# Kernel tuning notes

Hardware: AMD Instinct MI355X
Metric: run time of the kernel (lower is better)

Reference implementation:

```python
import jax, jax.numpy as jnp
import numpy as np

D_NODE = 100
D_HID = 300
EPS = 1e-5


def _gru_step_h0(x, W_ih, b_ih, b_hh):
    # Single torch-GRU step with h0 = 0 (seq len 1), so W_hh @ h0 vanishes
    # and only the hidden biases b_hh survive.
    gi = x @ W_ih.T + b_ih                      # [..., 3*H]
    H = D_HID
    r = jax.nn.sigmoid(gi[..., 0:H] + b_hh[0:H])
    z = jax.nn.sigmoid(gi[..., H:2 * H] + b_hh[H:2 * H])
    n = jnp.tanh(gi[..., 2 * H:3 * H] + r * b_hh[2 * H:3 * H])
    return (1.0 - z) * n                        # h' = (1-z)*n + z*0


def setup_inputs() -> dict:
    key = jax.random.key(0)
    ks = jax.random.split(key, 20)
    B, T, Lq, N = 128, 512, 256, 256
    s = 0.02
    inp = {
        "nodes": jax.random.normal(ks[0], (B * N, D_NODE), jnp.float32),
        "context_rep": jax.random.normal(ks[1], (B, Lq, D_HID), jnp.float32),
        "dia_triples": jax.random.randint(ks[2], (B, T, 3), 0, N, jnp.int64 if jax.config.jax_enable_x64 else jnp.int32),
        "node_number": N,
        # mean_trans: Linear(100, 300)
        "W_mean": s * jax.random.normal(ks[3], (D_HID, D_NODE), jnp.float32),
        "b_mean": jnp.zeros((D_HID,), jnp.float32),
        # bidirectional GRU(300 -> 300); h0=0 so W_hh drops out, keep biases
        "W_ih_f": s * jax.random.normal(ks[4], (3 * D_HID, D_HID), jnp.float32),
        "b_ih_f": s * jax.random.normal(ks[5], (3 * D_HID,), jnp.float32),
        "b_hh_f": s * jax.random.normal(ks[6], (3 * D_HID,), jnp.float32),
        "W_ih_b": s * jax.random.normal(ks[7], (3 * D_HID, D_HID), jnp.float32),
        "b_ih_b": s * jax.random.normal(ks[8], (3 * D_HID,), jnp.float32),
        "b_hh_b": s * jax.random.normal(ks[9], (3 * D_HID,), jnp.float32),
        # output_trans: Linear(600, 300) + tanh
        "W_out": s * jax.random.normal(ks[10], (D_HID, 2 * D_HID), jnp.float32),
        "b_out": jnp.zeros((D_HID,), jnp.float32),
        # trans_node_to_decoder_dim: Linear(100, 300)
        "W_node": s * jax.random.normal(ks[11], (D_HID, D_NODE), jnp.float32),
        "b_node": jnp.zeros((D_HID,), jnp.float32),
        # layernorm(300)
        "gamma": jnp.ones((D_HID,), jnp.float32),
        "beta": jnp.zeros((D_HID,), jnp.float32),
    }
    return inp


def reference(nodes, context_rep, dia_triples, node_number,
              W_mean, b_mean, W_ih_f, b_ih_f, b_hh_f,
              W_ih_b, b_ih_b, b_hh_b, W_out, b_out,
              W_node, b_node, gamma, beta):
    B = context_rep.shape[0]
    N = node_number
    T = dia_triples.shape[1]
    nodes3 = nodes.reshape(B, N, D_NODE)                        # per-dialogue node slices

    # gather head/tail nodes of each triple, mean-aggregate
    head = jnp.broadcast_to(dia_triples[:, :, 0][:, :, None], (B, T, D_NODE))
    tail = jnp.broadcast_to(dia_triples[:, :, -1][:, :, None], (B, T, D_NODE))
    gh = jnp.take_along_axis(nodes3, head, axis=1)              # [B,T,100]
    gt = jnp.take_along_axis(nodes3, tail, axis=1)
    tri_mean = 0.5 * (gh + gt)

    x = tri_mean @ W_mean.T + b_mean                            # [B,T,300] GRU inputs (len-1 paths)

    # bidirectional GRU, one step each direction from h0=0
    h_f = _gru_step_h0(x, W_ih_f, b_ih_f, b_hh_f)
    h_b = _gru_step_h0(x, W_ih_b, b_ih_b, b_hh_b)
    hidden = jnp.concatenate([h_f, h_b], axis=-1)               # [B,T,600]

    hid_ = jnp.tanh(hidden @ W_out.T + b_out)                   # [B,T,300]

    # attention: alpha = softmax(query @ hidden^T, -1).sum(0)
    scores = jnp.einsum("bld,btd->blt", context_rep, hid_)
    alpha = jax.nn.softmax(scores, axis=-1).sum(axis=1)         # [B,T]
    rep = jnp.einsum("bt,btd->bd", alpha, hid_)                 # [B,300]

    mu = rep.mean(axis=-1, keepdims=True)
    var = rep.var(axis=-1, keepdims=True)
    path_feature = (rep - mu) * jax.lax.rsqrt(var + EPS) * gamma + beta
    # dropout is identity in eval mode

    node_feature = nodes3 @ W_node.T + b_node                   # [B,N,300]
    node_mask = jnp.zeros((B, 1, N), dtype=bool)                # equal lengths -> no padding
    return path_feature, node_feature, node_mask
```

## Files before the change

### kernel.cpp

```cpp
#include <hip/hip_runtime.h>
#include <math.h>

#define D_NODE 100
#define D_HID  300
static const int TSEQ = 512, LQn = 256, NNODE = 256;

typedef unsigned int u32;
typedef unsigned short u16;
typedef __attribute__((ext_vector_type(8))) short bf16x8;
typedef __attribute__((ext_vector_type(4))) float f32x4;

__device__ __forceinline__ float bflo(u32 u){ return __uint_as_float(u << 16); }
__device__ __forceinline__ float bfhi(u32 u){ return __uint_as_float(u & 0xffff0000u); }
__device__ __forceinline__ float bf2f(u16 v){ return __uint_as_float(((u32)v) << 16); }
__device__ __forceinline__ u16 f2bf(float f){
    u32 u = __float_as_uint(f);
    return (u16)((u + 0x7fffu + ((u >> 16) & 1u)) >> 16);
}
__device__ __forceinline__ u32 pack_bf(float lo, float hi){
    return ((u32)f2bf(lo)) | (((u32)f2bf(hi)) << 16);
}
__device__ __forceinline__ void gload_lds16(const void* g, void* l){
    __builtin_amdgcn_global_load_lds(
        (const __attribute__((address_space(1))) u32*)g,
        (__attribute__((address_space(3))) u32*)l, 16, 0, 0);
}
__device__ __forceinline__ float fsig(float x){
    return __builtin_amdgcn_rcpf(1.f + __expf(-x));
}
__device__ __forceinline__ float ftanh(float x){
    return 1.f - 2.f*__builtin_amdgcn_rcpf(1.f + __expf(2.f*x));
}

__global__ __launch_bounds__(128)
void k0_prep(const float* __restrict__ Wm, const float* __restrict__ bm,
             const float* __restrict__ Wihf, const float* __restrict__ bihf, const float* __restrict__ bhhf,
             const float* __restrict__ Wihb, const float* __restrict__ bihb, const float* __restrict__ bhhb,
             u16* __restrict__ W4bf, float* __restrict__ bc, float* __restrict__ bhhn)
{
    int j = blockIdx.x, g = blockIdx.y, dir = blockIdx.z;
    int tid = threadIdx.x;
    u16* wout = W4bf + ((size_t)((dir*3+g)*320 + j))*128;
    if (j >= D_HID) {
        wout[tid] = 0;
        if (tid == 0) { bc[(dir*3+g)*320 + j] = 0.f; if (g==2) bhhn[dir*320+j] = 0.f; }
        return;
    }
    const float* Wih = dir ? Wihb : Wihf;
    const float* bih = dir ? bihb : bihf;
    const float* bhh = dir ? bhhb : bhhf;
    const float* wrow = Wih + (size_t)(g*D_HID + j)*D_HID;
    int k = tid;
    float s = 0.f;
    if (k < D_NODE)
        for (int q = 0; q < D_HID; ++q)
            s = fmaf(wrow[q], Wm[q*D_NODE + k], s);
    wout[k] = f2bf(k < D_NODE ? s : 0.f);

    __shared__ float red[128];
    float p = 0.f;
    for (int q = tid; q < D_HID; q += 128) p = fmaf(bm[q], wrow[q], p);
    red[tid] = p;
    __syncthreads();
    for (int off = 64; off > 0; off >>= 1) {
        if (tid < off) red[tid] += red[tid + off];
        __syncthreads();
    }
    if (tid == 0) {
        float base = bih[g*D_HID + j] + red[0];
        if (g < 2) base += bhh[g*D_HID + j];
        bc[(dir*3+g)*320 + j] = base;
        if (g == 2) bhhn[dir*320 + j] = bhh[2*D_HID + j];
    }
}

__global__ __launch_bounds__(256)
void kW(const float* __restrict__ Wout, const float* __restrict__ Wnode,
        u16* __restrict__ Woutbf, u16* __restrict__ Wnbf)
{
    int idx = blockIdx.x*256 + threadIdx.x;
    if (idx < 384*608) {
        int j = idx / 608, k = idx % 608;
        float v = (j < D_HID && k < 600) ? Wout[(size_t)j*600 + k] : 0.f;
        Woutbf[idx] = f2bf(v);
    } else {
        int i2 = idx - 384*608;
        if (i2 < 320*128) {
            int j = i2 >> 7, k = i2 & 127;
            float v = (j < D_HID && k < D_NODE) ? Wnode[(size_t)j*D_NODE + k] : 0.f;
            Wnbf[i2] = f2bf(v);
        }
    }
}

__global__ __launch_bounds__(256)
void kA(const float* __restrict__ nodes, const int* __restrict__ trip,
        u32* __restrict__ Abf, u32* __restrict__ Nbf)
{
    int gid = blockIdx.x*256 + threadIdx.x;
    if (gid < 65536) {
        int b = gid >> 9;
        int hidx = trip[(size_t)gid*3];
        int tidx = trip[(size_t)gid*3 + 2];
        const float4* nh = (const float4*)(nodes + ((size_t)b*NNODE + hidx)*D_NODE);
        const float4* nt = (const float4*)(nodes + ((size_t)b*NNODE + tidx)*D_NODE);
        u32* ar = Abf + (size_t)gid*64;
        #pragma unroll 5
        for (int i = 0; i < 25; ++i) {
            float4 a = nh[i], c = nt[i];
            ar[i*2]   = pack_bf(0.5f*(a.x+c.x), 0.5f*(a.y+c.y));
            ar[i*2+1] = pack_bf(0.5f*(a.z+c.z), 0.5f*(a.w+c.w));
        }
        #pragma unroll
        for (int i = 50; i < 64; ++i) ar[i] = 0;
    } else {
        int r = gid - 65536;
        if (r < 32768) {
            const float4* nr = (const float4*)(nodes + (size_t)r*D_NODE);
            u32* ar = Nbf + (size_t)r*64;
            #pragma unroll 5
            for (int i = 0; i < 25; ++i) {
                float4 a = nr[i];
                ar[i*2]   = pack_bf(a.x, a.y);
                ar[i*2+1] = pack_bf(a.z, a.w);
            }
            #pragma unroll
            for (int i = 50; i < 64; ++i) ar[i] = 0;
        }
    }
}

__global__ __launch_bounds__(256)
void kC(const float* __restrict__ ctx, u32* __restrict__ Cbf)
{
    int idx = blockIdx.x*256 + threadIdx.x;
    int r = idx / 160, cp = idx % 160;
    int col = cp*2;
    u32 v = 0;
    if (col < D_HID) {
        float2 f = *(const float2*)(ctx + (size_t)r*D_HID + col);
        v = pack_bf(f.x, f.y);
    }
    Cbf[(size_t)r*160 + cp] = v;
}

__global__ __launch_bounds__(256)
void k1_gru(const u16* __restrict__ Abf, const u16* __restrict__ W4bf,
            const float* __restrict__ bc, const float* __restrict__ bhhn,
            u16* __restrict__ H)
{
    __shared__ char smem[16384];
    int tid = threadIdx.x;
    int lane = tid & 63, w = tid >> 6;
    int l15 = lane & 15, lq = lane >> 4;
    int m0 = blockIdx.x * 64;
    int dir = blockIdx.y / 5;
    int jg = blockIdx.y % 5;
    int j0w = jg*64 + w*16;

    bf16x8 bfr[3][4];
    const u16* Wb = W4bf + (size_t)dir*3*320*128;
    #pragma unroll
    for (int g = 0; g < 3; ++g)
        #pragma unroll
        for (int ks = 0; ks < 4; ++ks)
            bfr[g][ks] = *(const bf16x8*)(Wb + ((size_t)(g*320 + j0w + l15))*128 + ks*32 + lq*8);

    #pragma unroll
    for (int ks = 0; ks < 4; ++ks) {
        const u16* g = Abf + ((size_t)(m0 + w*16 + l15))*128 + ks*32 + lq*8;
        gload_lds16(g, smem + (size_t)((w*4 + ks)*64)*16);
    }
    __syncthreads();

    f32x4 acc[4][3];
    #pragma unroll
    for (int ms = 0; ms < 4; ++ms)
        #pragma unroll
        for (int g = 0; g < 3; ++g)
            acc[ms][g] = (f32x4){0.f,0.f,0.f,0.f};

    #pragma unroll
    for (int ms = 0; ms < 4; ++ms)
        #pragma unroll
        for (int ks = 0; ks < 4; ++ks) {
            bf16x8 a = *(const bf16x8*)(smem + (size_t)(((ms*4+ks)*64 + lane))*16);
            acc[ms][0] = __builtin_amdgcn_mfma_f32_16x16x32_bf16(a, bfr[0][ks], acc[ms][0], 0,0,0);
            acc[ms][1] = __builtin_amdgcn_mfma_f32_16x16x32_bf16(a, bfr[1][ks], acc[ms][1], 0,0,0);
            acc[ms][2] = __builtin_amdgcn_mfma_f32_16x16x32_bf16(a, bfr[2][ks], acc[ms][2], 0,0,0);
        }

    int j = j0w + l15;
    float bcr = bc[(dir*3+0)*320 + j];
    float bcz = bc[(dir*3+1)*320 + j];
    float bcn = bc[(dir*3+2)*320 + j];
    float bn2 = bhhn[dir*320 + j];
    bool ok = (j < D_HID);
    #pragma unroll
    for (int ms = 0; ms < 4; ++ms)
        #pragma unroll
        for (int i = 0; i < 4; ++i) {
            float r = fsig(acc[ms][0][i] + bcr);
            float z = fsig(acc[ms][1][i] + bcz);
            float n = ftanh(acc[ms][2][i] + bcn + r*bn2);
            float h = (1.f - z)*n;
            if (ok) H[(size_t)(m0 + ms*16 + lq*4 + i)*608 + dir*D_HID + j] = f2bf(h);
        }
}

__global__ __launch_bounds__(256, 2)
void k2_out(const u16* __restrict__ H, const u16* __restrict__ Woutbf,
            const float* __restrict__ bout, u16* __restrict__ Hid)
{
    __shared__ char smem[40960];
    int tid = threadIdx.x;
    int lane = tid & 63, w = tid >> 6;
    int l15 = lane & 15, lq = lane >> 4;
    int m0 = blockIdx.x * 64;
    int j0 = blockIdx.y * 128;
    int jA = j0 + w*16, jB = j0 + 64 + w*16;

    bf16x8 bA[19], bB[19];
    #pragma unroll
    for (int ks = 0; ks < 19; ++ks) {
        bA[ks] = *(const bf16x8*)(Woutbf + ((size_t)(jA + l15))*608 + ks*32 + lq*8);
        bB[ks] = *(const bf16x8*)(Woutbf + ((size_t)(jB + l15))*608 + ks*32 + lq*8);
    }
    f32x4 acc[4][2];
    #pragma unroll
    for (int ms = 0; ms < 4; ++ms) { acc[ms][0] = (f32x4){0,0,0,0}; acc[ms][1] = (f32x4){0,0,0,0}; }

    #pragma unroll
    for (int c = 0; c < 2; ++c) {
        const int kb = c ? 10 : 0;
        const int nks = c ? 9 : 10;
        #pragma unroll
        for (int kk = 0; kk < 10; ++kk)
            if (kk < nks) {
                const u16* g = H + ((size_t)(m0 + w*16 + l15))*608 + (kb+kk)*32 + lq*8;
                gload_lds16(g, smem + (size_t)((w*10 + kk)*64)*16);
            }
        __syncthreads();
        #pragma unroll
        for (int ms = 0; ms < 4; ++ms)
            #pragma unroll
            for (int kk = 0; kk < 10; ++kk)
                if (kk < nks) {
                    bf16x8 a = *(const bf16x8*)(smem + (size_t)(((ms*10+kk)*64 + lane))*16);
                    acc[ms][0] = __builtin_amdgcn_mfma_f32_16x16x32_bf16(a, bA[kb+kk], acc[ms][0], 0,0,0);
                    acc[ms][1] = __builtin_amdgcn_mfma_f32_16x16x32_bf16(a, bB[kb+kk], acc[ms][1], 0,0,0);
                }
        __syncthreads();
    }

    #pragma unroll
    for (int jj = 0; jj < 2; ++jj) {
        int j = (jj ? jB : jA) + l15;
        if (j < 320) {
            bool real = (j < D_HID);
            float bo = real ? bout[j] : 0.f;
            #pragma unroll
            for (int ms = 0; ms < 4; ++ms)
                #pragma unroll
                for (int i = 0; i < 4; ++i) {
                    u16 v = real ? f2bf(ftanh(acc[ms][jj][i] + bo)) : (u16)0;
                    Hid[(size_t)(m0 + ms*16 + lq*4 + i)*320 + j] = v;
                }
        }
    }
}

__global__ __launch_bounds__(256, 2)
void k3_attn(const u16* __restrict__ Cbf, const u16* __restrict__ Hid,
             float* __restrict__ alphap)
{
    __shared__ char smemA[4096];
    __shared__ char smemB[32768];
    __shared__ float rmax[64*4], rsum[64*4];
    int tid = threadIdx.x;
    int lane = tid & 63, w = tid >> 6;
    int l15 = lane & 15, lq = lane >> 4;
    int b = blockIdx.y;
    int mblk = blockIdx.x;
    const u16* Ab = Cbf + ((size_t)b*LQn + mblk*64)*320;
    const u16* Bb = Hid + ((size_t)b*TSEQ)*320;

    f32x4 acc[4][8];
    #pragma unroll
    for (int ms = 0; ms < 4; ++ms)
        #pragma unroll
        for (int g = 0; g < 8; ++g)
            acc[ms][g] = (f32x4){0,0,0,0};

    for (int ks = 0; ks < 10; ++ks) {
        gload_lds16(Ab + ((size_t)(w*16 + l15))*320 + ks*32 + lq*8,
                    smemA + (size_t)(w*64)*16);
        #pragma unroll
        for (int i = 0; i < 8; ++i) {
            int nt = w*8 + i;
            gload_lds16(Bb + ((size_t)(nt*16 + l15))*320 + ks*32 + lq*8,
                        smemB + (size_t)(nt*64)*16);
        }
        __syncthreads();
        bf16x8 afr[4];
        #pragma unroll
        for (int ms = 0; ms < 4; ++ms)
            afr[ms] = *(const bf16x8*)(smemA + (size_t)((ms*64 + lane))*16);
        #pragma unroll
        for (int i = 0; i < 8; ++i) {
            bf16x8 bfr = *(const bf16x8*)(smemB + (size_t)(((w*8+i)*64 + lane))*16);
            #pragma unroll
            for (int ms = 0; ms < 4; ++ms)
                acc[ms][i] = __builtin_amdgcn_mfma_f32_16x16x32_bf16(afr[ms], bfr, acc[ms][i], 0,0,0);
        }
        __syncthreads();
    }

    #pragma unroll
    for (int ms = 0; ms < 4; ++ms)
        #pragma unroll
        for (int i = 0; i < 4; ++i) {
            float m = acc[ms][0][i];
            #pragma unroll
            for (int g = 1; g < 8; ++g) m = fmaxf(m, acc[ms][g][i]);
            m = fmaxf(m, __shfl_xor(m, 1));
            m = fmaxf(m, __shfl_xor(m, 2));
            m = fmaxf(m, __shfl_xor(m, 4));
            m = fmaxf(m, __shfl_xor(m, 8));
            if (l15 == 0) rmax[(ms*16 + lq*4 + i)*4 + w] = m;
        }
    __syncthreads();
    float mfin[4][4];
    #pragma unroll
    for (int ms = 0; ms < 4; ++ms)
        #pragma unroll
        for (int i = 0; i < 4; ++i) {
            float4 mv = *(const float4*)&rmax[(ms*16 + lq*4 + i)*4];
            mfin[ms][i] = fmaxf(fmaxf(mv.x, mv.y), fmaxf(mv.z, mv.w));
        }
    #pragma unroll
    for (int ms = 0; ms < 4; ++ms)
        #pragma unroll
        for (int i = 0; i < 4; ++i) {
            float s = 0.f;
            #pragma unroll
            for (int g = 0; g < 8; ++g) {
                float e = __expf(acc[ms][g][i] - mfin[ms][i]);
                acc[ms][g][i] = e;
                s += e;
            }
            s += __shfl_xor(s, 1);
            s += __shfl_xor(s, 2);
            s += __shfl_xor(s, 4);
            s += __shfl_xor(s, 8);
            if (l15 == 0) rsum[(ms*16 + lq*4 + i)*4 + w] = s;
        }
    __syncthreads();
    float inv[4][4];
    #pragma unroll
    for (int ms = 0; ms < 4; ++ms)
        #pragma unroll
        for (int i = 0; i < 4; ++i) {
            float4 sv = *(const float4*)&rsum[(ms*16 + lq*4 + i)*4];
            inv[ms][i] = __builtin_amdgcn_rcpf(sv.x + sv.y + sv.z + sv.w);
        }
    float* ap = alphap + ((size_t)b*4 + mblk)*TSEQ;
    #pragma unroll
    for (int g = 0; g < 8; ++g) {
        float c = 0.f;
        #pragma unroll
        for (int ms = 0; ms < 4; ++ms)
            #pragma unroll
            for (int i = 0; i < 4; ++i)
                c = fmaf(acc[ms][g][i], inv[ms][i], c);
        c += __shfl_xor(c, 16);
        c += __shfl_xor(c, 32);
        if (lq == 0) ap[w*128 + g*16 + l15] = c;
    }
}

__global__ __launch_bounds__(320)
void k4_rep(const float* __restrict__ alphap, const u16* __restrict__ Hid,
            const float* __restrict__ gamma, const float* __restrict__ beta,
            float* __restrict__ outP)
{
    __shared__ float al[512];
    __shared__ float rs[5], rss[5];
    int tid = threadIdx.x, b = blockIdx.x;
    const float* ap = alphap + (size_t)b*4*TSEQ;
    for (int i = tid; i < 512; i += 320)
        al[i] = ap[i] + ap[512 + i] + ap[1024 + i] + ap[1536 + i];
    __syncthreads();
    float acc = 0.f;
    if (tid < D_HID) {
        const u16* hp = Hid + (size_t)b*TSEQ*320 + tid;
        #pragma unroll 8
        for (int t = 0; t < TSEQ; ++t)
            acc = fmaf(al[t], bf2f(hp[(size_t)t*320]), acc);
    }
    float v = (tid < D_HID) ? acc : 0.f;
    float s = v, q = v*v;
    #pragma unroll
    for (int off = 32; off > 0; off >>= 1) { s += __shfl_xor(s, off, 64); q += __shfl_xor(q, off, 64); }
    if ((tid & 63) == 0) { rs[tid >> 6] = s; rss[tid >> 6] = q; }
    __syncthreads();
    float S = rs[0]+rs[1]+rs[2]+rs[3]+rs[4];
    float Q = rss[0]+rss[1]+rss[2]+rss[3]+rss[4];
    float mu = S * (1.f/300.f);
    float var = Q * (1.f/300.f) - mu*mu;
    if (tid < D_HID)
        outP[(size_t)b*D_HID + tid] = (acc - mu) * rsqrtf(var + 1e-5f) * gamma[tid] + beta[tid];
}

__global__ __launch_bounds__(256)
void k5_node(const u16* __restrict__ Nbf, const u16* __restrict__ Wnbf,
             const float* __restrict__ bn, float* __restrict__ outN)
{
    __shared__ char smem[16384];
    int tid = threadIdx.x;
    int lane = tid & 63, w = tid >> 6;
    int l15 = lane & 15, lq = lane >> 4;
    int m0 = blockIdx.x * 64;
    int j0w = blockIdx.y*64 + w*16;

    bf16x8 bw[4];
    #pragma unroll
    for (int ks = 0; ks < 4; ++ks)
        bw[ks] = *(const bf16x8*)(Wnbf + ((size_t)(j0w + l15))*128 + ks*32 + lq*8);

    #pragma unroll
    for (int ks = 0; ks < 4; ++ks) {
        const u16* g = Nbf + ((size_t)(m0 + w*16 + l15))*128 + ks*32 + lq*8;
        gload_lds16(g, smem + (size_t)((w*4 + ks)*64)*16);
    }
    __syncthreads();

    f32x4 acc[4];
    #pragma unroll
    for (int ms = 0; ms < 4; ++ms) acc[ms] = (f32x4){0,0,0,0};
    #pragma unroll
    for (int ms = 0; ms < 4; ++ms)
        #pragma unroll
        for (int ks = 0; ks < 4; ++ks) {
            bf16x8 a = *(const bf16x8*)(smem + (size_t)(((ms*4+ks)*64 + lane))*16);
            acc[ms] = __builtin_amdgcn_mfma_f32_16x16x32_bf16(a, bw[ks], acc[ms], 0,0,0);
        }

    int j = j0w + l15;
    if (j < D_HID) {
        float bo = bn[j];
        #pragma unroll
        for (int ms = 0; ms < 4; ++ms)
            #pragma unroll
            for (int i = 0; i < 4; ++i)
                outN[(size_t)(m0 + ms*16 + lq*4 + i)*D_HID + j] = acc[ms][i] + bo;
    }
}

extern "C" void kernel_launch(void* const* d_in, const int* in_sizes, int n_in,
                              void* d_out, int out_size, void* d_ws, size_t ws_size,
                              hipStream_t stream) {
    const float* nodes  = (const float*)d_in[0];
    const float* ctx    = (const float*)d_in[1];
    const int*   trip   = (const int*)d_in[2];
    const float* Wm     = (const float*)d_in[4];
    const float* bm     = (const float*)d_in[5];
    const float* Wihf   = (const float*)d_in[6];
    const float* bihf   = (const float*)d_in[7];
    const float* bhhf   = (const float*)d_in[8];
    const float* Wihb   = (const float*)d_in[9];
    const float* bihb   = (const float*)d_in[10];
    const float* bhhb   = (const float*)d_in[11];
    const float* Wout   = (const float*)d_in[12];
    const float* bout   = (const float*)d_in[13];
    const float* Wnode  = (const float*)d_in[14];
    const float* bnode  = (const float*)d_in[15];
    const float* gamma  = (const float*)d_in[16];
    const float* beta   = (const float*)d_in[17];
    float* out = (float*)d_out;

    char* ws = (char*)d_ws;
    u16*   W4bf   = (u16*)(ws);
    u16*   Woutbf = (u16*)(ws + 491520);
    u16*   Wnbf   = (u16*)(ws + 958464);
    float* bc     = (float*)(ws + 1040384);
    float* bhhn   = (float*)(ws + 1048064);
    char*  Hbase  = ws + 1050624;
    u16*   H      = (u16*)Hbase;
    u32*   Cbf    = (u32*)(Hbase + 33554432ull);
    char*  hidbase = Hbase + 79691776ull;
    u16*   Hid    = (u16*)hidbase;
    u32*   Abf    = (u32*)hidbase;
    u32*   Nbf    = (u32*)(hidbase + 16777216ull);
    float* alphap = (float*)(ws + 122685440ull);

    k0_prep<<<dim3(320,3,2), 128, 0, stream>>>(Wm,bm,Wihf,bihf,bhhf,Wihb,bihb,bhhb,W4bf,bc,bhhn);
    kW     <<<1072, 256, 0, stream>>>(Wout,Wnode,Woutbf,Wnbf);
    kA     <<<384,  256, 0, stream>>>(nodes,trip,Abf,Nbf);
    k1_gru <<<dim3(1024,10), 256, 0, stream>>>((const u16*)Abf,W4bf,bc,bhhn,H);
    k5_node<<<dim3(512,5),   256, 0, stream>>>((const u16*)Nbf,Wnbf,bnode,out + 38400);
    k2_out <<<dim3(1024,3),  256, 0, stream>>>(H,Woutbf,bout,Hid);
    kC     <<<20480, 256, 0, stream>>>(ctx, Cbf);
    k3_attn<<<dim3(4,128),   256, 0, stream>>>((const u16*)Cbf, Hid, alphap);
    k4_rep <<<128,           320, 0, stream>>>(alphap,Hid,gamma,beta,out);
    hipMemsetAsync(out + 38400 + 9830400, 0, 32768*sizeof(float), stream);
}
```

Baseline: 443.4 us.

## Fuse GRU step and output projection into one kernel via LDS-resident hidden

```diff
diff --git a/kernel.cpp b/kernel.cpp
--- a/kernel.cpp
+++ b/kernel.cpp
@@ -144,129 +144,118 @@
     Cbf[(size_t)r*160 + cp] = v;
 }
 
-__global__ __launch_bounds__(256)
-void k1_gru(const u16* __restrict__ Abf, const u16* __restrict__ W4bf,
-            const float* __restrict__ bc, const float* __restrict__ bhhn,
-            u16* __restrict__ H)
-{
-    __shared__ char smem[16384];
+__global__ __launch_bounds__(512, 2)
+void k12_fused(const u16* __restrict__ Abf, const u16* __restrict__ W4bf,
+               const float* __restrict__ bc, const float* __restrict__ bhhn,
+               const u16* __restrict__ Woutbf, const float* __restrict__ bout,
+               u16* __restrict__ Hid)
+{
+    __shared__ __attribute__((aligned(16))) char smem[16384 + 64*616*2];
+    u16* HT = (u16*)(smem + 16384);
+    const int HTS = 616;
     int tid = threadIdx.x;
     int lane = tid & 63, w = tid >> 6;
     int l15 = lane & 15, lq = lane >> 4;
     int m0 = blockIdx.x * 64;
-    int dir = blockIdx.y / 5;
-    int jg = blockIdx.y % 5;
-    int j0w = jg*64 + w*16;
-
-    bf16x8 bfr[3][4];
-    const u16* Wb = W4bf + (size_t)dir*3*320*128;
-    #pragma unroll
-    for (int g = 0; g < 3; ++g)
-        #pragma unroll
-        for (int ks = 0; ks < 4; ++ks)
-            bfr[g][ks] = *(const bf16x8*)(Wb + ((size_t)(g*320 + j0w + l15))*128 + ks*32 + lq*8);
-
-    #pragma unroll
-    for (int ks = 0; ks < 4; ++ks) {
-        const u16* g = Abf + ((size_t)(m0 + w*16 + l15))*128 + ks*32 + lq*8;
-        gload_lds16(g, smem + (size_t)((w*4 + ks)*64)*16);
-    }
-    __syncthreads();
-
-    f32x4 acc[4][3];
-    #pragma unroll
-    for (int ms = 0; ms < 4; ++ms)
+    int mh = w >> 2, wq = w & 3;
+
+    #pragma unroll
+    for (int r = 0; r < 2; ++r) {
+        int p = w + 8*r;
+        int pm = p >> 2, pk = p & 3;
+        const u16* g = Abf + ((size_t)(m0 + pm*16 + l15))*128 + pk*32 + lq*8;
+        gload_lds16(g, smem + (size_t)(p*64)*16);
+    }
+    if (tid < 64) {
+        *(f32x4*)(HT + (size_t)tid*HTS + 600) = (f32x4){0.f,0.f,0.f,0.f};
+        *(f32x4*)(HT + (size_t)tid*HTS + 608) = (f32x4){0.f,0.f,0.f,0.f};
+    }
+    __syncthreads();
+
+    #pragma unroll
+    for (int st = 0; st < 10; ++st) {
+        const int dir = st / 5, jg = st % 5;
+        const int j0w = jg*64 + wq*16;
+        const int j = j0w + l15;
+        const u16* Wb = W4bf + (size_t)dir*3*320*128;
+        bf16x8 bfr[3][4];
         #pragma unroll
         for (int g = 0; g < 3; ++g)
-            acc[ms][g] = (f32x4){0.f,0.f,0.f,0.f};
-
-    #pragma unroll
-    for (int ms = 0; ms < 4; ++ms)
-        #pragma unroll
-        for (int ks = 0; ks < 4; ++ks) {
-            bf16x8 a = *(const bf16x8*)(smem + (size_t)(((ms*4+ks)*64 + lane))*16);
-            acc[ms][0] = __builtin_amdgcn_mfma_f32_16x16x32_bf16(a, bfr[0][ks], acc[ms][0], 0,0,0);
-            acc[ms][1] = __builtin_amdgcn_mfma_f32_16x16x32_bf16(a, bfr[1][ks], acc[ms][1], 0,0,0);
-            acc[ms][2] = __builtin_amdgcn_mfma_f32_16x16x32_bf16(a, bfr[2][ks], acc[ms][2], 0,0,0);
-        }
-
-    int j = j0w + l15;
-    float bcr = bc[(dir*3+0)*320 + j];
-    float bcz = bc[(dir*3+1)*320 + j];
-    float bcn = bc[(dir*3+2)*320 + j];
-    float bn2 = bhhn[dir*320 + j];
-    bool ok = (j < D_HID);
-    #pragma unroll
-    for (int ms = 0; ms < 4; ++ms)
-        #pragma unroll
-        for (int i = 0; i < 4; ++i) {
-            float r = fsig(acc[ms][0][i] + bcr);
-            float z = fsig(acc[ms][1][i] + bcz);
-            float n = ftanh(acc[ms][2][i] + bcn + r*bn2);
-            float h = (1.f - z)*n;
-            if (ok) H[(size_t)(m0 + ms*16 + lq*4 + i)*608 + dir*D_HID + j] = f2bf(h);
-        }
-}
-
-__global__ __launch_bounds__(256, 2)
-void k2_out(const u16* __restrict__ H, const u16* __restrict__ Woutbf,
-            const float* __restrict__ bout, u16* __restrict__ Hid)
-{
-    __shared__ char smem[40960];
-    int tid = threadIdx.x;
-    int lane = tid & 63, w = tid >> 6;
-    int l15 = lane & 15, lq = lane >> 4;
-    int m0 = blockIdx.x * 64;
-    int j0 = blockIdx.y * 128;
-    int jA = j0 + w*16, jB = j0 + 64 + w*16;
-
-    bf16x8 bA[19], bB[19];
+            #pragma unroll
+            for (int ks = 0; ks < 4; ++ks)
+                bfr[g][ks] = *(const bf16x8*)(Wb + ((size_t)(g*320 + j0w + l15))*128 + ks*32 + lq*8);
+
+        f32x4 acc[2][3];
+        #pragma unroll
+        for (int ms = 0; ms < 2; ++ms)
+            #pragma unroll
+            for (int g = 0; g < 3; ++g)
+                acc[ms][g] = (f32x4){0.f,0.f,0.f,0.f};
+
+        #pragma unroll
+        for (int ms = 0; ms < 2; ++ms)
+            #pragma unroll
+            for (int ks = 0; ks < 4; ++ks) {
+                bf16x8 a = *(const bf16x8*)(smem + (size_t)((((mh*2+ms)*4+ks)*64 + lane))*16);
+                acc[ms][0] = __builtin_amdgcn_mfma_f32_16x16x32_bf16(a, bfr[0][ks], acc[ms][0], 0,0,0);
+                acc[ms][1] = __builtin_amdgcn_mfma_f32_16x16x32_bf16(a, bfr[1][ks], acc[ms][1], 0,0,0);
+                acc[ms][2] = __builtin_amdgcn_mfma_f32_16x16x32_bf16(a, bfr[2][ks], acc[ms][2], 0,0,0);
+            }
+
+        float bcr = bc[(dir*3+0)*320 + j];
+        float bcz = bc[(dir*3+1)*320 + j];
+        float bcn = bc[(dir*3+2)*320 + j];
+        float bn2 = bhhn[dir*320 + j];
+        bool ok = (j < D_HID);
+        int cb = dir*D_HID + j;
+        #pragma unroll
+        for (int ms = 0; ms < 2; ++ms)
+            #pragma unroll
+            for (int i = 0; i < 4; ++i) {
+                float r = fsig(acc[ms][0][i] + bcr);
+                float z = fsig(acc[ms][1][i] + bcz);
+                float n = ftanh(acc[ms][2][i] + bcn + r*bn2);
+                float h = (1.f - z)*n;
+                if (ok) HT[(size_t)(mh*32 + ms*16 + lq*4 + i)*HTS + cb] = f2bf(h);
+            }
+    }
+    __syncthreads();
+
+    int jcb = wq*80;
+    f32x4 acc2[2][5];
+    #pragma unroll
+    for (int ms = 0; ms < 2; ++ms)
+        #pragma unroll
+        for (int jj = 0; jj < 5; ++jj)
+            acc2[ms][jj] = (f32x4){0.f,0.f,0.f,0.f};
+
     #pragma unroll
     for (int ks = 0; ks < 19; ++ks) {
-        bA[ks] = *(const bf16x8*)(Woutbf + ((size_t)(jA + l15))*608 + ks*32 + lq*8);
-        bB[ks] = *(const bf16x8*)(Woutbf + ((size_t)(jB + l15))*608 + ks*32 + lq*8);
-    }
-    f32x4 acc[4][2];
-    #pragma unroll
-    for (int ms = 0; ms < 4; ++ms) { acc[ms][0] = (f32x4){0,0,0,0}; acc[ms][1] = (f32x4){0,0,0,0}; }
-
-    #pragma unroll
-    for (int c = 0; c < 2; ++c) {
-        const int kb = c ? 10 : 0;
-        const int nks = c ? 9 : 10;
-        #pragma unroll
-        for (int kk = 0; kk < 10; ++kk)
-            if (kk < nks) {
-                const u16* g = H + ((size_t)(m0 + w*16 + l15))*608 + (kb+kk)*32 + lq*8;
-                gload_lds16(g, smem + (size_t)((w*10 + kk)*64)*16);
+        bf16x8 bb[5];
+        #pragma unroll
+        for (int jj = 0; jj < 5; ++jj)
+            bb[jj] = *(const bf16x8*)(Woutbf + ((size_t)(jcb + jj*16 + l15))*608 + ks*32 + lq*8);
+        bf16x8 a0 = *(const bf16x8*)(HT + (size_t)(mh*32 +      l15)*HTS + ks*32 + lq*8);
+        bf16x8 a1 = *(const bf16x8*)(HT + (size_t)(mh*32 + 16 + l15)*HTS + ks*32 + lq*8);
+        #pragma unroll
+        for (int jj = 0; jj < 5; ++jj) {
+            acc2[0][jj] = __builtin_amdgcn_mfma_f32_16x16x32_bf16(a0, bb[jj], acc2[0][jj], 0,0,0);
+            acc2[1][jj] = __builtin_amdgcn_mfma_f32_16x16x32_bf16(a1, bb[jj], acc2[1][jj], 0,0,0);
+        }
+    }
+
+    #pragma unroll
+    for (int jj = 0; jj < 5; ++jj) {
+        int j = jcb + jj*16 + l15;
+        bool real = (j < D_HID);
+        float bo = real ? bout[j] : 0.f;
+        #pragma unroll
+        for (int ms = 0; ms < 2; ++ms)
+            #pragma unroll
+            for (int i = 0; i < 4; ++i) {
+                u16 v = real ? f2bf(ftanh(acc2[ms][jj][i] + bo)) : (u16)0;
+                Hid[(size_t)(m0 + mh*32 + ms*16 + lq*4 + i)*320 + j] = v;
             }
-        __syncthreads();
-        #pragma unroll
-        for (int ms = 0; ms < 4; ++ms)
-            #pragma unroll
-            for (int kk = 0; kk < 10; ++kk)
-                if (kk < nks) {
-                    bf16x8 a = *(const bf16x8*)(smem + (size_t)(((ms*10+kk)*64 + lane))*16);
-                    acc[ms][0] = __builtin_amdgcn_mfma_f32_16x16x32_bf16(a, bA[kb+kk], acc[ms][0], 0,0,0);
-                    acc[ms][1] = __builtin_amdgcn_mfma_f32_16x16x32_bf16(a, bB[kb+kk], acc[ms][1], 0,0,0);
-                }
-        __syncthreads();
-    }
-
-    #pragma unroll
-    for (int jj = 0; jj < 2; ++jj) {
-        int j = (jj ? jB : jA) + l15;
-        if (j < 320) {
-            bool real = (j < D_HID);
-            float bo = real ? bout[j] : 0.f;
-            #pragma unroll
-            for (int ms = 0; ms < 4; ++ms)
-                #pragma unroll
-                for (int i = 0; i < 4; ++i) {
-                    u16 v = real ? f2bf(ftanh(acc[ms][jj][i] + bo)) : (u16)0;
-                    Hid[(size_t)(m0 + ms*16 + lq*4 + i)*320 + j] = v;
-                }
-        }
     }
 }
 
@@ -485,23 +474,19 @@
     u16*   Wnbf   = (u16*)(ws + 958464);
     float* bc     = (float*)(ws + 1040384);
     float* bhhn   = (float*)(ws + 1048064);
-    char*  Hbase  = ws + 1050624;
-    u16*   H      = (u16*)Hbase;
-    u32*   Cbf    = (u32*)(Hbase + 33554432ull);
-    char*  hidbase = Hbase + 79691776ull;
-    u16*   Hid    = (u16*)hidbase;
-    u32*   Abf    = (u32*)hidbase;
-    u32*   Nbf    = (u32*)(hidbase + 16777216ull);
-    float* alphap = (float*)(ws + 122685440ull);
+    u32*   Abf    = (u32*)(ws + 1050624);
+    u32*   Nbf    = (u32*)(ws + 17827840ull);
+    u32*   Cbf    = (u32*)(ws + 26216448ull);
+    u16*   Hid    = (u16*)(ws + 47187968ull);
+    float* alphap = (float*)(ws + 89131008ull);
 
     k0_prep<<<dim3(320,3,2), 128, 0, stream>>>(Wm,bm,Wihf,bihf,bhhf,Wihb,bihb,bhhb,W4bf,bc,bhhn);
-    kW     <<<1072, 256, 0, stream>>>(Wout,Wnode,Woutbf,Wnbf);
-    kA     <<<384,  256, 0, stream>>>(nodes,trip,Abf,Nbf);
-    k1_gru <<<dim3(1024,10), 256, 0, stream>>>((const u16*)Abf,W4bf,bc,bhhn,H);
-    k5_node<<<dim3(512,5),   256, 0, stream>>>((const u16*)Nbf,Wnbf,bnode,out + 38400);
-    k2_out <<<dim3(1024,3),  256, 0, stream>>>(H,Woutbf,bout,Hid);
-    kC     <<<20480, 256, 0, stream>>>(ctx, Cbf);
-    k3_attn<<<dim3(4,128),   256, 0, stream>>>((const u16*)Cbf, Hid, alphap);
-    k4_rep <<<128,           320, 0, stream>>>(alphap,Hid,gamma,beta,out);
+    kW      <<<1072, 256, 0, stream>>>(Wout,Wnode,Woutbf,Wnbf);
+    kA      <<<384,  256, 0, stream>>>(nodes,trip,Abf,Nbf);
+    kC      <<<20480, 256, 0, stream>>>(ctx, Cbf);
+    k12_fused<<<1024, 512, 0, stream>>>((const u16*)Abf,W4bf,bc,bhhn,Woutbf,bout,Hid);
+    k5_node <<<dim3(512,5),  256, 0, stream>>>((const u16*)Nbf,Wnbf,bnode,out + 38400);
+    k3_attn <<<dim3(4,128),  256, 0, stream>>>((const u16*)Cbf, Hid, alphap);
+    k4_rep  <<<128,          320, 0, stream>>>(alphap,Hid,gamma,beta,out);
     hipMemsetAsync(out + 38400 + 9830400, 0, 32768*sizeof(float), stream);
 }
```

Result: slower. 461.5 us (+4.1%).

## Restructure GRU and output GEMMs into half-batch passes with register-held A tiles

Applied to the files above, without the earlier changes.

```diff
diff --git a/kernel.cpp b/kernel.cpp
--- a/kernel.cpp
+++ b/kernel.cpp
@@ -10,8 +10,6 @@
 typedef __attribute__((ext_vector_type(8))) short bf16x8;
 typedef __attribute__((ext_vector_type(4))) float f32x4;
 
-__device__ __forceinline__ float bflo(u32 u){ return __uint_as_float(u << 16); }
-__device__ __forceinline__ float bfhi(u32 u){ return __uint_as_float(u & 0xffff0000u); }
 __device__ __forceinline__ float bf2f(u16 v){ return __uint_as_float(((u32)v) << 16); }
 __device__ __forceinline__ u16 f2bf(float f){
     u32 u = __float_as_uint(f);
@@ -79,12 +77,16 @@
         u16* __restrict__ Woutbf, u16* __restrict__ Wnbf)
 {
     int idx = blockIdx.x*256 + threadIdx.x;
-    if (idx < 384*608) {
-        int j = idx / 608, k = idx % 608;
-        float v = (j < D_HID && k < 600) ? Wout[(size_t)j*600 + k] : 0.f;
+    if (idx < 320*640) {
+        int j = idx / 640, k = idx % 640;
+        float v = 0.f;
+        if (j < D_HID) {
+            if (k < D_HID)                 v = Wout[(size_t)j*600 + k];
+            else if (k >= 320 && k < 620)  v = Wout[(size_t)j*600 + (k - 20)];
+        }
         Woutbf[idx] = f2bf(v);
     } else {
-        int i2 = idx - 384*608;
+        int i2 = idx - 320*640;
         if (i2 < 320*128) {
             int j = i2 >> 7, k = i2 & 127;
             float v = (j < D_HID && k < D_NODE) ? Wnode[(size_t)j*D_NODE + k] : 0.f;
@@ -144,27 +146,16 @@
     Cbf[(size_t)r*160 + cp] = v;
 }
 
-__global__ __launch_bounds__(256)
+__global__ __launch_bounds__(256, 2)
 void k1_gru(const u16* __restrict__ Abf, const u16* __restrict__ W4bf,
             const float* __restrict__ bc, const float* __restrict__ bhhn,
             u16* __restrict__ H)
 {
-    __shared__ char smem[16384];
+    __shared__ __attribute__((aligned(16))) char smem[16384];
     int tid = threadIdx.x;
     int lane = tid & 63, w = tid >> 6;
     int l15 = lane & 15, lq = lane >> 4;
     int m0 = blockIdx.x * 64;
-    int dir = blockIdx.y / 5;
-    int jg = blockIdx.y % 5;
-    int j0w = jg*64 + w*16;
-
-    bf16x8 bfr[3][4];
-    const u16* Wb = W4bf + (size_t)dir*3*320*128;
-    #pragma unroll
-    for (int g = 0; g < 3; ++g)
-        #pragma unroll
-        for (int ks = 0; ks < 4; ++ks)
-            bfr[g][ks] = *(const bf16x8*)(Wb + ((size_t)(g*320 + j0w + l15))*128 + ks*32 + lq*8);
 
     #pragma unroll
     for (int ks = 0; ks < 4; ++ks) {
@@ -173,100 +164,116 @@
     }
     __syncthreads();
 
-    f32x4 acc[4][3];
-    #pragma unroll
-    for (int ms = 0; ms < 4; ++ms)
+    bf16x8 af[4][4];
+    #pragma unroll
+    for (int ms = 0; ms < 4; ++ms)
+        #pragma unroll
+        for (int ks = 0; ks < 4; ++ks)
+            af[ms][ks] = *(const bf16x8*)(smem + (size_t)(((ms*4+ks)*64 + lane))*16);
+
+    #pragma unroll
+    for (int st = 0; st < 10; ++st) {
+        const int dir = (st < 5) ? 0 : 1;
+        const int jg  = (st < 5) ? st : st - 5;
+        const int j0w = jg*64 + w*16;
+        const int j = j0w + l15;
+        const u16* Wb = W4bf + (size_t)dir*3*320*128;
+
+        bf16x8 bfr[3][4];
         #pragma unroll
         for (int g = 0; g < 3; ++g)
-            acc[ms][g] = (f32x4){0.f,0.f,0.f,0.f};
-
-    #pragma unroll
-    for (int ms = 0; ms < 4; ++ms)
-        #pragma unroll
-        for (int ks = 0; ks < 4; ++ks) {
-            bf16x8 a = *(const bf16x8*)(smem + (size_t)(((ms*4+ks)*64 + lane))*16);
-            acc[ms][0] = __builtin_amdgcn_mfma_f32_16x16x32_bf16(a, bfr[0][ks], acc[ms][0], 0,0,0);
-            acc[ms][1] = __builtin_amdgcn_mfma_f32_16x16x32_bf16(a, bfr[1][ks], acc[ms][1], 0,0,0);
-            acc[ms][2] = __builtin_amdgcn_mfma_f32_16x16x32_bf16(a, bfr[2][ks], acc[ms][2], 0,0,0);
-        }
-
-    int j = j0w + l15;
-    float bcr = bc[(dir*3+0)*320 + j];
-    float bcz = bc[(dir*3+1)*320 + j];
-    float bcn = bc[(dir*3+2)*320 + j];
-    float bn2 = bhhn[dir*320 + j];
-    bool ok = (j < D_HID);
-    #pragma unroll
-    for (int ms = 0; ms < 4; ++ms)
-        #pragma unroll
-        for (int i = 0; i < 4; ++i) {
-            float r = fsig(acc[ms][0][i] + bcr);
-            float z = fsig(acc[ms][1][i] + bcz);
-            float n = ftanh(acc[ms][2][i] + bcn + r*bn2);
-            float h = (1.f - z)*n;
-            if (ok) H[(size_t)(m0 + ms*16 + lq*4 + i)*608 + dir*D_HID + j] = f2bf(h);
-        }
+            #pragma unroll
+            for (int ks = 0; ks < 4; ++ks)
+                bfr[g][ks] = *(const bf16x8*)(Wb + ((size_t)(g*320 + j0w + l15))*128 + ks*32 + lq*8);
+
+        f32x4 acc[4][3];
+        #pragma unroll
+        for (int ms = 0; ms < 4; ++ms)
+            #pragma unroll
+            for (int g = 0; g < 3; ++g)
+                acc[ms][g] = (f32x4){0.f,0.f,0.f,0.f};
+
+        #pragma unroll
+        for (int ms = 0; ms < 4; ++ms)
+            #pragma unroll
+            for (int ks = 0; ks < 4; ++ks) {
+                acc[ms][0] = __builtin_amdgcn_mfma_f32_16x16x32_bf16(af[ms][ks], bfr[0][ks], acc[ms][0], 0,0,0);
+                acc[ms][1] = __builtin_amdgcn_mfma_f32_16x16x32_bf16(af[ms][ks], bfr[1][ks], acc[ms][1], 0,0,0);
+                acc[ms][2] = __builtin_amdgcn_mfma_f32_16x16x32_bf16(af[ms][ks], bfr[2][ks], acc[ms][2], 0,0,0);
+            }
+
+        float bcr = bc[(dir*3+0)*320 + j];
+        float bcz = bc[(dir*3+1)*320 + j];
+        float bcn = bc[(dir*3+2)*320 + j];
+        float bn2 = bhhn[dir*320 + j];
+        bool ok = (j < D_HID);
+        #pragma unroll
+        for (int ms = 0; ms < 4; ++ms)
+            #pragma unroll
+            for (int i = 0; i < 4; ++i) {
+                float r = fsig(acc[ms][0][i] + bcr);
+                float z = fsig(acc[ms][1][i] + bcz);
+                float n = ftanh(acc[ms][2][i] + bcn + r*bn2);
+                float h = (1.f - z)*n;
+                H[(size_t)(m0 + ms*16 + lq*4 + i)*640 + dir*320 + j] = ok ? f2bf(h) : (u16)0;
+            }
+    }
 }
 
 __global__ __launch_bounds__(256, 2)
 void k2_out(const u16* __restrict__ H, const u16* __restrict__ Woutbf,
             const float* __restrict__ bout, u16* __restrict__ Hid)
 {
-    __shared__ char smem[40960];
+    __shared__ __attribute__((aligned(16))) char smem[8192];
     int tid = threadIdx.x;
     int lane = tid & 63, w = tid >> 6;
     int l15 = lane & 15, lq = lane >> 4;
     int m0 = blockIdx.x * 64;
-    int j0 = blockIdx.y * 128;
-    int jA = j0 + w*16, jB = j0 + 64 + w*16;
-
-    bf16x8 bA[19], bB[19];
-    #pragma unroll
-    for (int ks = 0; ks < 19; ++ks) {
-        bA[ks] = *(const bf16x8*)(Woutbf + ((size_t)(jA + l15))*608 + ks*32 + lq*8);
-        bB[ks] = *(const bf16x8*)(Woutbf + ((size_t)(jB + l15))*608 + ks*32 + lq*8);
-    }
-    f32x4 acc[4][2];
-    #pragma unroll
-    for (int ms = 0; ms < 4; ++ms) { acc[ms][0] = (f32x4){0,0,0,0}; acc[ms][1] = (f32x4){0,0,0,0}; }
-
-    #pragma unroll
-    for (int c = 0; c < 2; ++c) {
-        const int kb = c ? 10 : 0;
-        const int nks = c ? 9 : 10;
-        #pragma unroll
-        for (int kk = 0; kk < 10; ++kk)
-            if (kk < nks) {
-                const u16* g = H + ((size_t)(m0 + w*16 + l15))*608 + (kb+kk)*32 + lq*8;
-                gload_lds16(g, smem + (size_t)((w*10 + kk)*64)*16);
+
+    f32x4 acc[4][5];
+    #pragma unroll
+    for (int ms = 0; ms < 4; ++ms)
+        #pragma unroll
+        for (int jj = 0; jj < 5; ++jj)
+            acc[ms][jj] = (f32x4){0.f,0.f,0.f,0.f};
+
+    for (int c = 0; c < 10; ++c) {
+        #pragma unroll
+        for (int r = 0; r < 2; ++r) {
+            int p = w*2 + r, pm = p >> 1, pk = p & 1;
+            gload_lds16(H + ((size_t)(m0 + pm*16 + l15))*640 + c*64 + pk*32 + lq*8,
+                        smem + (size_t)(p*64)*16);
+        }
+        __syncthreads();
+        #pragma unroll
+        for (int pk = 0; pk < 2; ++pk) {
+            bf16x8 bb[5];
+            #pragma unroll
+            for (int jj = 0; jj < 5; ++jj)
+                bb[jj] = *(const bf16x8*)(Woutbf + ((size_t)(w*80 + jj*16 + l15))*640 + c*64 + pk*32 + lq*8);
+            #pragma unroll
+            for (int ms = 0; ms < 4; ++ms) {
+                bf16x8 a = *(const bf16x8*)(smem + (size_t)(((ms*2+pk)*64 + lane))*16);
+                #pragma unroll
+                for (int jj = 0; jj < 5; ++jj)
+                    acc[ms][jj] = __builtin_amdgcn_mfma_f32_16x16x32_bf16(a, bb[jj], acc[ms][jj], 0,0,0);
             }
+        }
         __syncthreads();
-        #pragma unroll
-        for (int ms = 0; ms < 4; ++ms)
-            #pragma unroll
-            for (int kk = 0; kk < 10; ++kk)
-                if (kk < nks) {
-                    bf16x8 a = *(const bf16x8*)(smem + (size_t)(((ms*10+kk)*64 + lane))*16);
-                    acc[ms][0] = __builtin_amdgcn_mfma_f32_16x16x32_bf16(a, bA[kb+kk], acc[ms][0], 0,0,0);
-                    acc[ms][1] = __builtin_amdgcn_mfma_f32_16x16x32_bf16(a, bB[kb+kk], acc[ms][1], 0,0,0);
-                }
-        __syncthreads();
-    }
-
-    #pragma unroll
-    for (int jj = 0; jj < 2; ++jj) {
-        int j = (jj ? jB : jA) + l15;
-        if (j < 320) {
-            bool real = (j < D_HID);
-            float bo = real ? bout[j] : 0.f;
-            #pragma unroll
-            for (int ms = 0; ms < 4; ++ms)
-                #pragma unroll
-                for (int i = 0; i < 4; ++i) {
-                    u16 v = real ? f2bf(ftanh(acc[ms][jj][i] + bo)) : (u16)0;
-                    Hid[(size_t)(m0 + ms*16 + lq*4 + i)*320 + j] = v;
-                }
-        }
+    }
+
+    #pragma unroll
+    for (int jj = 0; jj < 5; ++jj) {
+        int j = w*80 + jj*16 + l15;
+        bool real = (j < D_HID);
+        float bo = real ? bout[j] : 0.f;
+        #pragma unroll
+        for (int ms = 0; ms < 4; ++ms)
+            #pragma unroll
+            for (int i = 0; i < 4; ++i) {
+                u16 v = real ? f2bf(ftanh(acc[ms][jj][i] + bo)) : (u16)0;
+                Hid[(size_t)(m0 + ms*16 + lq*4 + i)*320 + j] = v;
+            }
     }
 }
 
@@ -482,26 +489,30 @@
     char* ws = (char*)d_ws;
     u16*   W4bf   = (u16*)(ws);
     u16*   Woutbf = (u16*)(ws + 491520);
-    u16*   Wnbf   = (u16*)(ws + 958464);
-    float* bc     = (float*)(ws + 1040384);
-    float* bhhn   = (float*)(ws + 1048064);
-    char*  Hbase  = ws + 1050624;
-    u16*   H      = (u16*)Hbase;
-    u32*   Cbf    = (u32*)(Hbase + 33554432ull);
-    char*  hidbase = Hbase + 79691776ull;
-    u16*   Hid    = (u16*)hidbase;
-    u32*   Abf    = (u32*)hidbase;
-    u32*   Nbf    = (u32*)(hidbase + 16777216ull);
-    float* alphap = (float*)(ws + 122685440ull);
+    u16*   Wnbf   = (u16*)(ws + 901120);
+    float* bc     = (float*)(ws + 983040);
+    float* bhhn   = (float*)(ws + 990720);
+    u32*   Abf    = (u32*)(ws + 1048576);
+    u32*   Nbf    = (u32*)(ws + 17825792ull);
+    u16*   Hhalf  = (u16*)(ws + 26214400ull);
+    u32*   Cbf    = (u32*)(ws + 26214400ull);
+    u16*   Hid    = (u16*)(ws + 68157440ull);
+    float* alphap = (float*)(ws + 110100480ull);
 
     k0_prep<<<dim3(320,3,2), 128, 0, stream>>>(Wm,bm,Wihf,bihf,bhhf,Wihb,bihb,bhhb,W4bf,bc,bhhn);
-    kW     <<<1072, 256, 0, stream>>>(Wout,Wnode,Woutbf,Wnbf);
+    kW     <<<960,  256, 0, stream>>>(Wout,Wnode,Woutbf,Wnbf);
     kA     <<<384,  256, 0, stream>>>(nodes,trip,Abf,Nbf);
-    k1_gru <<<dim3(1024,10), 256, 0, stream>>>((const u16*)Abf,W4bf,bc,bhhn,H);
-    k5_node<<<dim3(512,5),   256, 0, stream>>>((const u16*)Nbf,Wnbf,bnode,out + 38400);
-    k2_out <<<dim3(1024,3),  256, 0, stream>>>(H,Woutbf,bout,Hid);
+
+    for (int h = 0; h < 2; ++h) {
+        const u16* Ah   = (const u16*)Abf + (size_t)h*32768*128;
+        u16*       Hidh = Hid + (size_t)h*32768*320;
+        k1_gru<<<512, 256, 0, stream>>>(Ah, W4bf, bc, bhhn, Hhalf);
+        k2_out<<<512, 256, 0, stream>>>(Hhalf, Woutbf, bout, Hidh);
+    }
+
+    k5_node<<<dim3(512,5), 256, 0, stream>>>((const u16*)Nbf,Wnbf,bnode,out + 38400);
     kC     <<<20480, 256, 0, stream>>>(ctx, Cbf);
-    k3_attn<<<dim3(4,128),   256, 0, stream>>>((const u16*)Cbf, Hid, alphap);
-    k4_rep <<<128,           320, 0, stream>>>(alphap,Hid,gamma,beta,out);
+    k3_attn<<<dim3(4,128), 256, 0, stream>>>((const u16*)Cbf, Hid, alphap);
+    k4_rep <<<128,         320, 0, stream>>>(alphap,Hid,gamma,beta,out);
     hipMemsetAsync(out + 38400 + 9830400, 0, 32768*sizeof(float), stream);
 }
```

New measurement: 446.3 us. Within noise of the previous version (+0.7%).
